# Kernel optimization log

Hardware: AMD Instinct MI355X
Metric: run time of the kernel (lower is better)

Reference implementation:

```python
import jax, jax.numpy as jnp
import numpy as np

B, LQ, LK, DQ, DK, DV = 8, 2048, 2048, 1024, 1024, 1024
TOP_K = 64
NEG_INF = float('-inf')


def setup_inputs() -> dict:
    key = jax.random.key(0)
    kq, kk, kv, km, kw = jax.random.split(key, 5)
    queries = jax.random.normal(kq, (B, LQ, DQ), dtype=jnp.float32)
    keys = jax.random.normal(kk, (B, LK, DK), dtype=jnp.float32)
    values = jax.random.normal(kv, (B, LK, DV), dtype=jnp.float32)
    mask = jax.random.randint(km, (B, LQ, LK), 0, 2, dtype=jnp.int32)
    # nn.Linear(query_dim, key_dim, bias=False) weight: [key_dim, query_dim]
    W = jax.random.normal(kw, (DK, DQ), dtype=jnp.float32) / np.sqrt(DQ)
    return {"queries": queries, "keys": keys, "values": values,
            "mask": mask, "W": W, "top_k": TOP_K}


def reference(queries, keys, values, mask, W, top_k):
    # scores = (queries @ W.T) @ keys^T  -> [B, LQ, LK]  (method='general')
    q_proj = jnp.einsum('bqd,kd->bqk', queries, W)  # [B, LQ, DK]
    scores = jnp.einsum('bqd,btd->bqt', q_proj, keys)  # [B, LQ, LK]
    scores = jnp.where(mask == 0, NEG_INF, scores)
    alphas = jax.nn.softmax(scores, axis=-1)
    alphas = jnp.where(jnp.isnan(alphas), 0.0, alphas)  # fully-masked rows -> 0
    # top-k: zero out non-top-k probabilities, then re-softmax over the
    # resulting tensor (zeros contribute exp(0)=1, matching torch semantics)
    _, idx = jax.lax.top_k(alphas, top_k)  # [B, LQ, top_k]
    b_idx = jnp.arange(alphas.shape[0])[:, None, None]
    q_idx = jnp.arange(alphas.shape[1])[None, :, None]
    topk_mask = jnp.zeros(alphas.shape, alphas.dtype).at[b_idx, q_idx, idx].set(1.0)
    alphas = jnp.where(topk_mask == 0, 0.0, alphas)
    alphas = jax.nn.softmax(alphas, axis=-1)
    alphas = jnp.where(jnp.isnan(alphas), 0.0, alphas)
    # dropout_rate = 0.0 -> identity
    return jnp.einsum('bqt,btd->bqd', alphas, values)  # [B, LQ, DV]
```

## Files before the change

### kernel.cpp

```cpp
#include <hip/hip_runtime.h>
#include <math.h>

#define BATCH 8
#define SEQ   2048
#define DIM   1024
#define TOPK  64
#define NEGMASK -1e30f
#define CAND_THRESH 16.0f
#define CAP 28

typedef _Float16 f16;
typedef _Float16 f16x8 __attribute__((ext_vector_type(8)));
typedef float f32x4 __attribute__((ext_vector_type(4)));

__device__ __forceinline__ void async_load16(const void* g, void* l) {
  __builtin_amdgcn_global_load_lds(
      (const __attribute__((address_space(1))) void*)g,
      (__attribute__((address_space(3))) void*)l, 16, 0, 0);
}

__device__ __forceinline__ uint2 cvt4(float4 v) {
  union { f16 h[4]; uint2 u; } pk;
  pk.h[0] = (f16)v.x; pk.h[1] = (f16)v.y; pk.h[2] = (f16)v.z; pk.h[3] = (f16)v.w;
  return pk.u;
}

__global__ __launch_bounds__(256) void prep_kernel(
    const float* __restrict__ queries, const float* __restrict__ W,
    f16* __restrict__ q16, f16* __restrict__ w16) {
  const int blk = blockIdx.x;
  if (blk < 4096) {
    const float4* src = (const float4*)queries;
    uint2* dst = (uint2*)q16;
    const int base = blk * 1024 + threadIdx.x;
    float4 v0 = src[base];
    float4 v1 = src[base + 256];
    float4 v2 = src[base + 512];
    float4 v3 = src[base + 768];
    dst[base]       = cvt4(v0);
    dst[base + 256] = cvt4(v1);
    dst[base + 512] = cvt4(v2);
    dst[base + 768] = cvt4(v3);
  } else {
    const float4* src = (const float4*)W;
    uint2* dst = (uint2*)w16;
    const int base = (blk - 4096) * 1024 + threadIdx.x;
    float4 v0 = src[base];
    float4 v1 = src[base + 256];
    float4 v2 = src[base + 512];
    float4 v3 = src[base + 768];
    dst[base]       = cvt4(v0);
    dst[base + 256] = cvt4(v1);
    dst[base + 512] = cvt4(v2);
    dst[base + 768] = cvt4(v3);
  }
}


#define STAGEK(KOFF, BUF)                                                   \
  async_load16(srcA0 + (KOFF), smA + (BUF) * 8192 + wave * 2048);           \
  async_load16(srcA1 + (KOFF), smA + (BUF) * 8192 + wave * 2048 + 1024);    \
  async_load16(srcB0 + (KOFF), smB + (BUF) * 8192 + wave * 2048);           \
  async_load16(srcB1 + (KOFF), smB + (BUF) * 8192 + wave * 2048 + 1024);

#define GEMM_PROLOGUE(APTR, BPTR)                                           \
  const int tid = threadIdx.x;                                              \
  const int wave = tid >> 6, lane = tid & 63;                               \
  const int wm = (wave >> 1) * 64, wn = (wave & 1) * 64;                    \
  const int r0 = wave * 32 + (lane >> 2);                                   \
  const int c16 = (lane & 3) ^ ((r0 >> 1) & 3);                            \
  const f16* srcA0 = (APTR) + (size_t)(m0 + r0) * DIM + c16 * 8;           \
  const f16* srcA1 = (APTR) + (size_t)(m0 + r0 + 16) * DIM + c16 * 8;      \
  const f16* srcB0 = (BPTR) + (size_t)(n0 + r0) * DIM + c16 * 8;           \
  const f16* srcB1 = (BPTR) + (size_t)(n0 + r0 + 16) * DIM + c16 * 8;      \
  int offA[4], offB[4];                                                     \
  _Pragma("unroll")                                                         \
  for (int i = 0; i < 4; ++i) {                                             \
    int r = wm + i * 16 + (lane & 15);                                      \
    offA[i] = r * 64 + ((lane >> 4) ^ ((r >> 1) & 3)) * 16;                 \
    int rn = wn + i * 16 + (lane & 15);                                     \
    offB[i] = rn * 64 + ((lane >> 4) ^ ((rn >> 1) & 3)) * 16;               \
  }                                                                         \
  f32x4 acc[4][4];                                                          \
  _Pragma("unroll")                                                         \
  for (int i = 0; i < 4; ++i)                                               \
    _Pragma("unroll")                                                       \
    for (int j = 0; j < 4; ++j)                                             \
      acc[i][j] = (f32x4){0.f, 0.f, 0.f, 0.f};                              \
  STAGEK(0, 0)                                                              \
  STAGEK(32, 1)                                                             \
  asm volatile("s_waitcnt vmcnt(4)" ::: "memory");                          \
  __builtin_amdgcn_s_barrier();                                             \
  asm volatile("" ::: "memory");                                            \
  f16x8 af[4], bf[4];                                                       \
  _Pragma("unroll")                                                         \
  for (int i = 0; i < 4; ++i) {                                             \
    af[i] = *(const f16x8*)(smA + offA[i]);                                 \
    bf[i] = *(const f16x8*)(smB + offB[i]);                                 \
  }                                                                         \
  int cur = 0;                                                              \
  for (int k0 = 0; k0 < DIM; k0 += 32) {                                    \
    if (k0 + 64 < DIM) {                                                    \
      const int nx2 = cur >= 1 ? cur - 1 : cur + 2;          \
      STAGEK(k0 + 64, nx2)                                                  \
    }                                                                       \
    _Pragma("unroll")                                                       \
    for (int i = 0; i < 4; ++i)                                             \
      _Pragma("unroll")                                                     \
      for (int j = 0; j < 4; ++j)                                           \
        acc[i][j] = __builtin_amdgcn_mfma_f32_16x16x32_f16(                 \
            af[i], bf[j], acc[i][j], 0, 0, 0);                              \
    if (k0 + 64 < DIM) {                                                    \
      asm volatile("s_waitcnt vmcnt(4)" ::: "memory");                      \
    } else {                                                                \
      asm volatile("s_waitcnt vmcnt(0)" ::: "memory");                      \
    }                                                                       \
    __builtin_amdgcn_s_barrier();                                           \
    asm volatile("" ::: "memory");                                          \
    const int nxt = cur == 2 ? 0 : cur + 1;                                 \
    if (k0 + 32 < DIM) {                                                    \
      _Pragma("unroll")                                                     \
      for (int i = 0; i < 4; ++i) {                                         \
        af[i] = *(const f16x8*)(smA + nxt * 8192 + offA[i]);                \
        bf[i] = *(const f16x8*)(smB + nxt * 8192 + offB[i]);                \
      }                                                                     \
    }                                                                       \
    cur = nxt;                                                              \
  }

__global__ __launch_bounds__(256, 3) void gemm_qproj(
    const f16* __restrict__ A, const f16* __restrict__ Bw,
    f16* __restrict__ C,
    const float* __restrict__ keys, f16* __restrict__ k16,
    const float* __restrict__ values, float* __restrict__ partial) {
  __shared__ __align__(128) char smA[24576];
  __shared__ __align__(128) char smB[24576];
  if (blockIdx.x >= 5120) {
    const int bid = (int)blockIdx.x - 5120;
    int tc = bid >> 5;
    int b  = (bid >> 2) & 7;
    int dg = bid & 3;
    int d  = dg * 256 + threadIdx.x;
    const float* vp = values + ((size_t)b * SEQ + (size_t)tc * 64) * DIM + d;
    float s = 0.f;
    #pragma unroll 8
    for (int t = 0; t < 64; ++t) s += vp[(size_t)t * DIM];
    partial[((size_t)tc * BATCH + b) * DIM + d] = s;
    return;
  }
  if (blockIdx.x >= 1024) {
    const float4* src = (const float4*)keys;
    uint2* dst = (uint2*)k16;
    const int base = ((int)blockIdx.x - 1024) * 1024 + threadIdx.x;
    float4 v0 = src[base];
    float4 v1 = src[base + 256];
    float4 v2 = src[base + 512];
    float4 v3 = src[base + 768];
    dst[base]       = cvt4(v0);
    dst[base + 256] = cvt4(v1);
    dst[base + 512] = cvt4(v2);
    dst[base + 768] = cvt4(v3);
    return;
  }
  const int swz = ((int)blockIdx.x & 7) * 128 + ((int)blockIdx.x >> 3);
  const int m0 = (swz >> 3) * 128;
  const int n0 = (swz & 7) * 128;
  GEMM_PROLOGUE(A, Bw)
  const int cr = m0 + wm + (lane >> 4) * 4;
  const int cc = n0 + wn + (lane & 15);
  #pragma unroll
  for (int i = 0; i < 4; ++i)
    #pragma unroll
    for (int j = 0; j < 4; ++j)
      #pragma unroll
      for (int reg = 0; reg < 4; ++reg)
        C[(size_t)(cr + i * 16 + reg) * DIM + cc + j * 16] = (f16)acc[i][j][reg];
}

__global__ __launch_bounds__(256, 3) void gemm_scores(
    const f16* __restrict__ QP, const f16* __restrict__ K16,
    const int* __restrict__ mask,
    float2* __restrict__ cand,
    int* __restrict__ counts,
    const float* __restrict__ partial, float* __restrict__ colsum) {
  __shared__ __align__(128) char smA[24576];
  __shared__ __align__(128) char smB[24576];
  if (blockIdx.x >= 2048) {
    int idx = ((int)blockIdx.x - 2048) * 256 + threadIdx.x;
    float s = 0.f;
    #pragma unroll
    for (int tc = 0; tc < 32; ++tc) s += partial[(size_t)tc * 8192 + idx];
    colsum[idx] = s;
    return;
  }
  const int swz = ((int)blockIdx.x & 7) * 256 + ((int)blockIdx.x >> 3);
  const int m0 = (swz >> 4) * 128;
  const int n0 = (swz & 15) * 128;
  const int b  = m0 >> 11;
  const f16* Bk = K16 + (size_t)b * SEQ * DIM;
  GEMM_PROLOGUE(QP, Bk)

  const int g  = lane >> 4;
  const int lc = lane & 15;

  #pragma unroll
  for (int i = 0; i < 4; ++i)
    #pragma unroll
    for (int reg = 0; reg < 4; ++reg) {
      const int r = wm + i * 16 + g * 4 + reg;
      const int* mp = mask + (size_t)(m0 + r) * SEQ + n0 + wn + lc;
      int m0v = mp[0], m1v = mp[16], m2v = mp[32], m3v = mp[48];
      if (m0v == 0) acc[i][0][reg] = NEGMASK;
      if (m1v == 0) acc[i][1][reg] = NEGMASK;
      if (m2v == 0) acc[i][2][reg] = NEGMASK;
      if (m3v == 0) acc[i][3][reg] = NEGMASK;
    }

  float* hm = (float*)smA;
  #pragma unroll
  for (int i = 0; i < 4; ++i)
    #pragma unroll
    for (int reg = 0; reg < 4; ++reg) {
      const int r = wm + i * 16 + g * 4 + reg;
      float m4 = fmaxf(fmaxf(acc[i][0][reg], acc[i][1][reg]),
                       fmaxf(acc[i][2][reg], acc[i][3][reg]));
      #pragma unroll
      for (int off = 8; off >= 1; off >>= 1) m4 = fmaxf(m4, __shfl_xor(m4, off));
      if (lc == 0) hm[r * 2 + (wn >> 6)] = m4;
    }
  __syncthreads();

  const int pairbase = (n0 >> 7) * 2 + (wn >> 6);
  #pragma unroll
  for (int i = 0; i < 4; ++i)
    #pragma unroll
    for (int reg = 0; reg < 4; ++reg) {
      const int r = wm + i * 16 + g * 4 + reg;
      const float tm = fmaxf(hm[r * 2], hm[r * 2 + 1]);
      const float thresh = fmaxf(tm - CAND_THRESH, -1e29f);
      float2* slot = cand + ((size_t)(m0 + r) * 32 + pairbase) * CAP;
      int cnt = 0;
      #pragma unroll
      for (int j = 0; j < 4; ++j) {
        const float s = acc[i][j][reg];
        const bool c = s > thresh;
        const unsigned long long bal = __ballot(c);
        const int seg = (int)((bal >> (g * 16)) & 0xFFFFull);
        const int pos = cnt + __popc(seg & ((1 << lc) - 1));
        if (c && pos < CAP) {
          float2 e; e.x = s; e.y = __int_as_float(n0 + wn + j * 16 + lc);
          slot[pos] = e;
        }
        cnt += __popc(seg);
      }
      if (lc == 0) counts[(size_t)(m0 + r) * 32 + pairbase] = cnt < CAP ? cnt : CAP;
    }
}

__global__ __launch_bounds__(512) void topk_kernel(
    const float2* __restrict__ cand,
    const int*    __restrict__ counts,
    const float*  __restrict__ values,
    const float*  __restrict__ colsum,
    float* __restrict__ out)
{
  __shared__ float ssc[8][128];
  __shared__ int   sidx[8][128];
  const int wave = threadIdx.x >> 6;
  const int lane = threadIdx.x & 63;
  const int grow = blockIdx.x * 8 + wave;
  const int b    = grow >> 11;
  float* msc = ssc[wave];
  int*   mix = sidx[wave];

  int cnt_p = 0;
  if (lane < 32) cnt_p = counts[(size_t)grow * 32 + lane];
  const float2* myslots = cand + ((size_t)grow * 32 + lane) * CAP;

  float mv = -3e38f;
  for (int k = 0; k < cnt_p; ++k) mv = fmaxf(mv, myslots[k].x);
  #pragma unroll
  for (int off = 32; off > 0; off >>= 1) mv = fmaxf(mv, __shfl_xor(mv, off));
  const bool dead = (mv <= -1e29f);

  float total_g = 0.f;
  f32x4 oacc[4];
  #pragma unroll
  for (int j = 0; j < 4; ++j) oacc[j] = (f32x4){0.f, 0.f, 0.f, 0.f};
  const float* vbase = values + (size_t)b * SEQ * DIM;

  if (!dead) {
    const float thresh = mv - CAND_THRESH;
    int f = 0; float zp = 0.f;
    for (int k = 0; k < cnt_p; ++k) {
      float s = myslots[k].x;
      if (s > thresh) { ++f; zp += __expf(s - mv); }
    }
    int incl = f;
    #pragma unroll
    for (int off = 1; off < 64; off <<= 1) {
      int t = __shfl_up(incl, off);
      if (lane >= off) incl += t;
    }
    const int base = incl - f;
    const int F = __shfl(incl, 63);
    #pragma unroll
    for (int off = 32; off > 0; off >>= 1) zp += __shfl_xor(zp, off);
    const float Z = zp;
    int w = 0;
    for (int k = 0; k < cnt_p; ++k) {
      float2 cv = myslots[k];
      if (cv.x > thresh) {
        int p = base + w;
        if (p < 128) { msc[p] = cv.x; mix[p] = __float_as_int(cv.y); }
        ++w;
      }
    }
    asm volatile("s_waitcnt lgkmcnt(0)" ::: "memory");

    if (F <= TOPK) {
      for (int c = 0; c < F; ++c) {
        float g = expm1f(__expf(msc[c] - mv) / Z);
        total_g += g;
        const float* vrow = vbase + (size_t)mix[c] * DIM;
        #pragma unroll
        for (int j = 0; j < 4; ++j) {
          f32x4 v = *(const f32x4*)(vrow + j * 256 + lane * 4);
          #pragma unroll
          for (int e = 0; e < 4; ++e) oacc[j][e] = fmaf(g, v[e], oacc[j][e]);
        }
      }
    } else {
      const int nlist = F < 128 ? F : 128;
      for (int itk = 0; itk < TOPK; ++itk) {
        float bv = -3e38f; int bi = 1 << 30; int bsl = -1;
        #pragma unroll
        for (int h = 0; h < 2; ++h) {
          int sl = lane + h * 64;
          if (sl < nlist) {
            float v = msc[sl]; int id = mix[sl];
            if (v > bv || (v == bv && id < bi)) { bv = v; bi = id; bsl = sl; }
          }
        }
        #pragma unroll
        for (int off = 32; off > 0; off >>= 1) {
          float ov = __shfl_xor(bv, off);
          int   oi = __shfl_xor(bi, off);
          int   os = __shfl_xor(bsl, off);
          if (ov > bv || (ov == bv && oi < bi)) { bv = ov; bi = oi; bsl = os; }
        }
        if (bv <= -1e29f) break;
        float g = expm1f(__expf(bv - mv) / Z);
        total_g += g;
        const float* vrow = vbase + (size_t)bi * DIM;
        #pragma unroll
        for (int j = 0; j < 4; ++j) {
          f32x4 v = *(const f32x4*)(vrow + j * 256 + lane * 4);
          #pragma unroll
          for (int e = 0; e < 4; ++e) oacc[j][e] = fmaf(g, v[e], oacc[j][e]);
        }
        if (lane == 0) msc[bsl] = -3e38f;
        asm volatile("s_waitcnt lgkmcnt(0)" ::: "memory");
      }
    }
  }

  const float inv = 1.0f / (2048.0f + total_g);
  const float* cs = colsum + (size_t)b * DIM;
  float* orow = out + (size_t)grow * DIM;
  #pragma unroll
  for (int j = 0; j < 4; ++j) {
    f32x4 c = *(const f32x4*)(cs + j * 256 + lane * 4);
    f32x4 o;
    #pragma unroll
    for (int e = 0; e < 4; ++e) o[e] = (c[e] + oacc[j][e]) * inv;
    *(f32x4*)(orow + j * 256 + lane * 4) = o;
  }
}

extern "C" void kernel_launch(void* const* d_in, const int* in_sizes, int n_in,
                              void* d_out, int out_size, void* d_ws, size_t ws_size,
                              hipStream_t stream) {
  const float* queries = (const float*)d_in[0];
  const float* keys    = (const float*)d_in[1];
  const float* values  = (const float*)d_in[2];
  const int*   mask    = (const int*)d_in[3];
  const float* W       = (const float*)d_in[4];
  float* out = (float*)d_out;

  char* base = (char*)d_ws;
  float2* cand   = (float2*)base;
  f16*   q16     = (f16*)base;
  f16*   w16     = (f16*)(base + (size_t)32 * 1024 * 1024);
  int*   counts  = (int*)(base + (size_t)112 * 1024 * 1024);
  float* colsum  = (float*)(base + (size_t)118 * 1024 * 1024);
  float* partial = (float*)(base + (size_t)119 * 1024 * 1024);
  f16*   qp16    = (f16*)(base + (size_t)128 * 1024 * 1024);
  f16*   k16     = (f16*)(base + (size_t)160 * 1024 * 1024);

  prep_kernel<<<4352, 256, 0, stream>>>(queries, W, q16, w16);
  gemm_qproj<<<6144, 256, 0, stream>>>(q16, w16, qp16, keys, k16, values, partial);
  gemm_scores<<<2080, 256, 0, stream>>>(qp16, k16, mask, cand, counts,
                                        partial, colsum);
  topk_kernel<<<2048, 512, 0, stream>>>(cand, counts, values, colsum, out);
}
```

Measured before the change: 275.6 us.

## Shrink GEMM blocks to single-wave 64x64 tiles without barriers

Both GEMM kernels move from 256-thread blocks with 128x128 tiles to 64-thread single-wave blocks with 64x64 tiles. With one wave per block, the LDS pipeline no longer needs s_barrier, and the scores kernel's cross-wave row-max exchange through shared memory and __syncthreads is dropped. The candidate threshold is now taken from a per-64-column max instead of a per-128-column max. The change loses operand reuse across waves in LDS, roughly doubling global traffic per output, and quadruples block count.

```diff
diff --git a/kernel.cpp b/kernel.cpp
--- a/kernel.cpp
+++ b/kernel.cpp
@@ -58,29 +58,23 @@
 
 
 #define STAGEK(KOFF, BUF)                                                   \
-  async_load16(srcA0 + (KOFF), smA + (BUF) * 8192 + wave * 2048);           \
-  async_load16(srcA1 + (KOFF), smA + (BUF) * 8192 + wave * 2048 + 1024);    \
-  async_load16(srcB0 + (KOFF), smB + (BUF) * 8192 + wave * 2048);           \
-  async_load16(srcB1 + (KOFF), smB + (BUF) * 8192 + wave * 2048 + 1024);
-
-#define GEMM_PROLOGUE(APTR, BPTR)                                           \
-  const int tid = threadIdx.x;                                              \
-  const int wave = tid >> 6, lane = tid & 63;                               \
-  const int wm = (wave >> 1) * 64, wn = (wave & 1) * 64;                    \
-  const int r0 = wave * 32 + (lane >> 2);                                   \
-  const int c16 = (lane & 3) ^ ((r0 >> 1) & 3);                            \
-  const f16* srcA0 = (APTR) + (size_t)(m0 + r0) * DIM + c16 * 8;           \
-  const f16* srcA1 = (APTR) + (size_t)(m0 + r0 + 16) * DIM + c16 * 8;      \
-  const f16* srcB0 = (BPTR) + (size_t)(n0 + r0) * DIM + c16 * 8;           \
-  const f16* srcB1 = (BPTR) + (size_t)(n0 + r0 + 16) * DIM + c16 * 8;      \
-  int offA[4], offB[4];                                                     \
-  _Pragma("unroll")                                                         \
-  for (int i = 0; i < 4; ++i) {                                             \
-    int r = wm + i * 16 + (lane & 15);                                      \
-    offA[i] = r * 64 + ((lane >> 4) ^ ((r >> 1) & 3)) * 16;                 \
-    int rn = wn + i * 16 + (lane & 15);                                     \
-    offB[i] = rn * 64 + ((lane >> 4) ^ ((rn >> 1) & 3)) * 16;               \
-  }                                                                         \
+  async_load16(sA + 0 * 16384 + (KOFF), sm + (BUF) * 8192 + 0);             \
+  async_load16(sA + 1 * 16384 + (KOFF), sm + (BUF) * 8192 + 1024);          \
+  async_load16(sA + 2 * 16384 + (KOFF), sm + (BUF) * 8192 + 2048);          \
+  async_load16(sA + 3 * 16384 + (KOFF), sm + (BUF) * 8192 + 3072);          \
+  async_load16(sB + 0 * 16384 + (KOFF), sm + (BUF) * 8192 + 4096);          \
+  async_load16(sB + 1 * 16384 + (KOFF), sm + (BUF) * 8192 + 5120);          \
+  async_load16(sB + 2 * 16384 + (KOFF), sm + (BUF) * 8192 + 6144);          \
+  async_load16(sB + 3 * 16384 + (KOFF), sm + (BUF) * 8192 + 7168);
+
+#define GEMM_CORE(APTR, BPTR)                                               \
+  const int lane = threadIdx.x & 63;                                        \
+  const int l15 = lane & 15;                                                \
+  const int rx = lane >> 2;                                                 \
+  const int gsw = (lane & 3) ^ ((rx >> 1) & 3);                             \
+  const f16* sA = (APTR) + (size_t)(m0 + rx) * DIM + gsw * 8;               \
+  const f16* sB = (BPTR) + (size_t)(n0 + rx) * DIM + gsw * 8;               \
+  const int aoff = l15 * 64 + (((lane >> 4) ^ ((l15 >> 1) & 3)) * 16);      \
   f32x4 acc[4][4];                                                          \
   _Pragma("unroll")                                                         \
   for (int i = 0; i < 4; ++i)                                               \
@@ -90,13 +84,11 @@
   STAGEK(0, 0)                                                              \
   STAGEK(32, 1)                                                             \
   asm volatile("s_waitcnt vmcnt(4)" ::: "memory");                          \
-  __builtin_amdgcn_s_barrier();                                             \
-  asm volatile("" ::: "memory");                                            \
   f16x8 af[4], bf[4];                                                       \
   _Pragma("unroll")                                                         \
   for (int i = 0; i < 4; ++i) {                                             \
-    af[i] = *(const f16x8*)(smA + offA[i]);                                 \
-    bf[i] = *(const f16x8*)(smB + offB[i]);                                 \
+    af[i] = *(const f16x8*)(sm + aoff + i * 1024);                          \
+    bf[i] = *(const f16x8*)(sm + 4096 + aoff + i * 1024);                   \
   }                                                                         \
   int cur = 0;                                                              \
   for (int k0 = 0; k0 < DIM; k0 += 32) {                                    \
@@ -110,37 +102,35 @@
       for (int j = 0; j < 4; ++j)                                           \
         acc[i][j] = __builtin_amdgcn_mfma_f32_16x16x32_f16(                 \
             af[i], bf[j], acc[i][j], 0, 0, 0);                              \
-    if (k0 + 64 < DIM) {                                                    \
-      asm volatile("s_waitcnt vmcnt(4)" ::: "memory");                      \
-    } else {                                                                \
-      asm volatile("s_waitcnt vmcnt(0)" ::: "memory");                      \
-    }                                                                       \
-    __builtin_amdgcn_s_barrier();                                           \
-    asm volatile("" ::: "memory");                                          \
-    const int nxt = cur == 2 ? 0 : cur + 1;                                 \
     if (k0 + 32 < DIM) {                                                    \
+      if (k0 + 64 < DIM) {                                                  \
+        asm volatile("s_waitcnt vmcnt(4)" ::: "memory");                    \
+      } else {                                                              \
+        asm volatile("s_waitcnt vmcnt(0)" ::: "memory");                    \
+      }                                                                     \
+      const int nxt = cur == 2 ? 0 : cur + 1;                               \
       _Pragma("unroll")                                                     \
       for (int i = 0; i < 4; ++i) {                                         \
-        af[i] = *(const f16x8*)(smA + nxt * 8192 + offA[i]);                \
-        bf[i] = *(const f16x8*)(smB + nxt * 8192 + offB[i]);                \
+        af[i] = *(const f16x8*)(sm + nxt * 8192 + aoff + i * 1024);         \
+        bf[i] = *(const f16x8*)(sm + nxt * 8192 + 4096 + aoff + i * 1024);  \
       }                                                                     \
+      cur = nxt;                                                            \
     }                                                                       \
-    cur = nxt;                                                              \
-  }
-
-__global__ __launch_bounds__(256, 3) void gemm_qproj(
+  }
+
+__global__ __launch_bounds__(64, 2) void gemm_qproj(
     const f16* __restrict__ A, const f16* __restrict__ Bw,
     f16* __restrict__ C,
     const float* __restrict__ keys, f16* __restrict__ k16,
     const float* __restrict__ values, float* __restrict__ partial) {
-  __shared__ __align__(128) char smA[24576];
-  __shared__ __align__(128) char smB[24576];
-  if (blockIdx.x >= 5120) {
-    const int bid = (int)blockIdx.x - 5120;
-    int tc = bid >> 5;
-    int b  = (bid >> 2) & 7;
-    int dg = bid & 3;
-    int d  = dg * 256 + threadIdx.x;
+  __shared__ __align__(128) char sm[24576];
+  const int tid = threadIdx.x;
+  if (blockIdx.x >= 20480) {
+    const int bid = (int)blockIdx.x - 20480;
+    int tc = bid >> 7;
+    int b  = (bid >> 4) & 7;
+    int dg = bid & 15;
+    int d  = dg * 64 + tid;
     const float* vp = values + ((size_t)b * SEQ + (size_t)tc * 64) * DIM + d;
     float s = 0.f;
     #pragma unroll 8
@@ -148,26 +138,26 @@
     partial[((size_t)tc * BATCH + b) * DIM + d] = s;
     return;
   }
-  if (blockIdx.x >= 1024) {
+  if (blockIdx.x >= 4096) {
     const float4* src = (const float4*)keys;
     uint2* dst = (uint2*)k16;
-    const int base = ((int)blockIdx.x - 1024) * 1024 + threadIdx.x;
+    const int base = ((int)blockIdx.x - 4096) * 256 + tid;
     float4 v0 = src[base];
-    float4 v1 = src[base + 256];
-    float4 v2 = src[base + 512];
-    float4 v3 = src[base + 768];
+    float4 v1 = src[base + 64];
+    float4 v2 = src[base + 128];
+    float4 v3 = src[base + 192];
     dst[base]       = cvt4(v0);
-    dst[base + 256] = cvt4(v1);
-    dst[base + 512] = cvt4(v2);
-    dst[base + 768] = cvt4(v3);
+    dst[base + 64]  = cvt4(v1);
+    dst[base + 128] = cvt4(v2);
+    dst[base + 192] = cvt4(v3);
     return;
   }
-  const int swz = ((int)blockIdx.x & 7) * 128 + ((int)blockIdx.x >> 3);
-  const int m0 = (swz >> 3) * 128;
-  const int n0 = (swz & 7) * 128;
-  GEMM_PROLOGUE(A, Bw)
-  const int cr = m0 + wm + (lane >> 4) * 4;
-  const int cc = n0 + wn + (lane & 15);
+  const int swz = ((int)blockIdx.x & 7) * 512 + ((int)blockIdx.x >> 3);
+  const int m0 = (swz >> 4) * 64;
+  const int n0 = (swz & 15) * 64;
+  GEMM_CORE(A, Bw)
+  const int cr = m0 + (lane >> 4) * 4;
+  const int cc = n0 + l15;
   #pragma unroll
   for (int i = 0; i < 4; ++i)
     #pragma unroll
@@ -177,68 +167,50 @@
         C[(size_t)(cr + i * 16 + reg) * DIM + cc + j * 16] = (f16)acc[i][j][reg];
 }
 
-__global__ __launch_bounds__(256, 3) void gemm_scores(
+__global__ __launch_bounds__(64, 2) void gemm_scores(
     const f16* __restrict__ QP, const f16* __restrict__ K16,
     const int* __restrict__ mask,
     float2* __restrict__ cand,
     int* __restrict__ counts,
     const float* __restrict__ partial, float* __restrict__ colsum) {
-  __shared__ __align__(128) char smA[24576];
-  __shared__ __align__(128) char smB[24576];
-  if (blockIdx.x >= 2048) {
-    int idx = ((int)blockIdx.x - 2048) * 256 + threadIdx.x;
+  __shared__ __align__(128) char sm[24576];
+  if (blockIdx.x >= 8192) {
+    int idx = ((int)blockIdx.x - 8192) * 64 + threadIdx.x;
     float s = 0.f;
     #pragma unroll
     for (int tc = 0; tc < 32; ++tc) s += partial[(size_t)tc * 8192 + idx];
     colsum[idx] = s;
     return;
   }
-  const int swz = ((int)blockIdx.x & 7) * 256 + ((int)blockIdx.x >> 3);
-  const int m0 = (swz >> 4) * 128;
-  const int n0 = (swz & 15) * 128;
+  const int swz = ((int)blockIdx.x & 7) * 1024 + ((int)blockIdx.x >> 3);
+  const int m0 = (swz >> 5) * 64;
+  const int n0 = (swz & 31) * 64;
   const int b  = m0 >> 11;
   const f16* Bk = K16 + (size_t)b * SEQ * DIM;
-  GEMM_PROLOGUE(QP, Bk)
+  GEMM_CORE(QP, Bk)
 
   const int g  = lane >> 4;
-  const int lc = lane & 15;
+  const int lc = l15;
+  const int pairb = n0 >> 6;
 
   #pragma unroll
   for (int i = 0; i < 4; ++i)
     #pragma unroll
     for (int reg = 0; reg < 4; ++reg) {
-      const int r = wm + i * 16 + g * 4 + reg;
-      const int* mp = mask + (size_t)(m0 + r) * SEQ + n0 + wn + lc;
+      const int r = i * 16 + g * 4 + reg;
+      const size_t grow = (size_t)m0 + r;
+      const int* mp = mask + grow * SEQ + n0 + lc;
       int m0v = mp[0], m1v = mp[16], m2v = mp[32], m3v = mp[48];
       if (m0v == 0) acc[i][0][reg] = NEGMASK;
       if (m1v == 0) acc[i][1][reg] = NEGMASK;
       if (m2v == 0) acc[i][2][reg] = NEGMASK;
       if (m3v == 0) acc[i][3][reg] = NEGMASK;
-    }
-
-  float* hm = (float*)smA;
-  #pragma unroll
-  for (int i = 0; i < 4; ++i)
-    #pragma unroll
-    for (int reg = 0; reg < 4; ++reg) {
-      const int r = wm + i * 16 + g * 4 + reg;
       float m4 = fmaxf(fmaxf(acc[i][0][reg], acc[i][1][reg]),
                        fmaxf(acc[i][2][reg], acc[i][3][reg]));
       #pragma unroll
       for (int off = 8; off >= 1; off >>= 1) m4 = fmaxf(m4, __shfl_xor(m4, off));
-      if (lc == 0) hm[r * 2 + (wn >> 6)] = m4;
-    }
-  __syncthreads();
-
-  const int pairbase = (n0 >> 7) * 2 + (wn >> 6);
-  #pragma unroll
-  for (int i = 0; i < 4; ++i)
-    #pragma unroll
-    for (int reg = 0; reg < 4; ++reg) {
-      const int r = wm + i * 16 + g * 4 + reg;
-      const float tm = fmaxf(hm[r * 2], hm[r * 2 + 1]);
-      const float thresh = fmaxf(tm - CAND_THRESH, -1e29f);
-      float2* slot = cand + ((size_t)(m0 + r) * 32 + pairbase) * CAP;
+      const float thresh = fmaxf(m4 - CAND_THRESH, -1e29f);
+      float2* slot = cand + (grow * 32 + pairb) * CAP;
       int cnt = 0;
       #pragma unroll
       for (int j = 0; j < 4; ++j) {
@@ -248,12 +220,12 @@
         const int seg = (int)((bal >> (g * 16)) & 0xFFFFull);
         const int pos = cnt + __popc(seg & ((1 << lc) - 1));
         if (c && pos < CAP) {
-          float2 e; e.x = s; e.y = __int_as_float(n0 + wn + j * 16 + lc);
+          float2 e; e.x = s; e.y = __int_as_float(n0 + j * 16 + lc);
           slot[pos] = e;
         }
         cnt += __popc(seg);
       }
-      if (lc == 0) counts[(size_t)(m0 + r) * 32 + pairbase] = cnt < CAP ? cnt : CAP;
+      if (lc == 0) counts[grow * 32 + pairb] = cnt < CAP ? cnt : CAP;
     }
 }
 
@@ -399,8 +371,8 @@
   f16*   k16     = (f16*)(base + (size_t)160 * 1024 * 1024);
 
   prep_kernel<<<4352, 256, 0, stream>>>(queries, W, q16, w16);
-  gemm_qproj<<<6144, 256, 0, stream>>>(q16, w16, qp16, keys, k16, values, partial);
-  gemm_scores<<<2080, 256, 0, stream>>>(qp16, k16, mask, cand, counts,
-                                        partial, colsum);
+  gemm_qproj<<<24576, 64, 0, stream>>>(q16, w16, qp16, keys, k16, values, partial);
+  gemm_scores<<<8320, 64, 0, stream>>>(qp16, k16, mask, cand, counts,
+                                       partial, colsum);
   topk_kernel<<<2048, 512, 0, stream>>>(cand, counts, values, colsum, out);
 }
```

Result: slower. 405.7 us (+47.2%).
